# Optimization experiments

Hardware: AMD Instinct MI355X
Metric: run time of the kernel (lower is better)

## Reference

```python
import jax, jax.numpy as jnp
import numpy as np

N = 50000
E = 1600000
D_IN = 128
D_HID = 64
BN_EPS = 1e-5


def setup_inputs() -> dict:
    key = jax.random.key(0)
    ks = jax.random.split(key, 12)
    x = jax.random.normal(ks[0], (N, D_IN), dtype=jnp.float32)
    edge_index_sc = jax.random.randint(ks[1], (2, E), 0, N, dtype=jnp.int64)
    edge_weight_sc = jax.random.uniform(ks[2], (E,), dtype=jnp.float32)
    edge_index_fc = jax.random.randint(ks[3], (2, E), 0, N, dtype=jnp.int64)
    edge_weight_fc = jax.random.uniform(ks[4], (E,), dtype=jnp.float32)
    # learned parameters
    alpha = jnp.float32(0.5)
    W1 = jax.random.normal(ks[5], (D_IN, D_HID), dtype=jnp.float32) / np.sqrt(D_IN)
    b1 = jnp.zeros((D_HID,), dtype=jnp.float32)
    W2 = jax.random.normal(ks[6], (D_HID, D_HID), dtype=jnp.float32) / np.sqrt(D_HID)
    b2 = jnp.zeros((D_HID,), dtype=jnp.float32)
    gamma1 = jnp.ones((D_HID,), dtype=jnp.float32)
    beta1 = jnp.zeros((D_HID,), dtype=jnp.float32)
    gamma2 = jnp.ones((D_HID,), dtype=jnp.float32)
    beta2 = jnp.zeros((D_HID,), dtype=jnp.float32)
    return {"x": x, "edge_index_sc": edge_index_sc, "edge_weight_sc": edge_weight_sc,
            "edge_index_fc": edge_index_fc, "edge_weight_fc": edge_weight_fc,
            "alpha": alpha, "W1": W1, "b1": b1, "W2": W2, "b2": b2,
            "gamma1": gamma1, "beta1": beta1, "gamma2": gamma2, "beta2": beta2}


def _gcn_layer(h, W, b, src, dst, norm, n):
    # h: [N, d_in] -> [N, d_out]; PyG GCNConv: transform, then weighted scatter-add
    h = h @ W
    msg = h[src] * norm[:, None]                # [E+N, d_out] gather + scale
    out = jax.ops.segment_sum(msg, dst, num_segments=n)
    return out + b


def _bn_relu(h, gamma, beta):
    # BatchNorm1d (training-mode batch stats, biased variance) + ReLU
    mean = jnp.mean(h, axis=0)
    var = jnp.var(h, axis=0)
    h = (h - mean) * jax.lax.rsqrt(var + BN_EPS) * gamma + beta
    return jax.nn.relu(h)


def reference(x, edge_index_sc, edge_weight_sc, edge_index_fc, edge_weight_fc,
              alpha, W1, b1, W2, b2, gamma1, beta1, gamma2, beta2):
    n = x.shape[0]
    a = jax.nn.sigmoid(alpha)
    # mixed weights on SC topology (edge_index_fc unused, as in original)
    w_mix = a * edge_weight_sc + (1.0 - a) * edge_weight_fc
    # add self loops (weight 1) and compute symmetric GCN normalization
    loop = jnp.arange(n, dtype=edge_index_sc.dtype)
    src = jnp.concatenate([edge_index_sc[0], loop])
    dst = jnp.concatenate([edge_index_sc[1], loop])
    w = jnp.concatenate([w_mix, jnp.ones((n,), dtype=w_mix.dtype)])
    deg = jax.ops.segment_sum(w, dst, num_segments=n)
    dinv = jnp.where(deg > 0, jax.lax.rsqrt(jnp.maximum(deg, 1e-12)), 0.0)
    norm = dinv[src] * w * dinv[dst]
    h = _gcn_layer(x, W1, b1, src, dst, norm, n)
    h = _bn_relu(h, gamma1, beta1)
    h = _gcn_layer(h, W2, b2, src, dst, norm, n)
    h = _bn_relu(h, gamma2, beta2)
    return h  # dropout is identity in eval mode
```

## Files before the change

### kernel.cpp

```cpp
#include <hip/hip_runtime.h>
#include <hip/hip_fp16.h>
#include <math.h>

#define N_NODES 50000
#define N_EDGES 1600000
#define D_INF   128
#define D_HID   64
#define BN_EPS  1e-5f
#define NBINS   391
#define BINCAP  4608
#define EPB     6250
#define GEMM1B  3125
#define NPAIR   3125
#define NCOPY   64

struct SmGemm { float sw[D_INF * D_HID]; float sx[16 * D_INF]; };
struct SmBin  { int hcnt[NBINS]; int hbase[NBINS]; };
union SmPre { SmGemm g; SmBin a; };

__global__ __launch_bounds__(256) void k_pre(const float* __restrict__ wsc,
                                             const float* __restrict__ wfc,
                                             const int*   __restrict__ ei,
                                             const float* __restrict__ alpha,
                                             int* __restrict__ bin_cur,
                                             unsigned long long* __restrict__ binned,
                                             const float* __restrict__ x,
                                             const float* __restrict__ W,
                                             __half* __restrict__ ha,
                                             __half* __restrict__ hb) {
    __shared__ SmPre sm;
    int t = threadIdx.x;
    if (blockIdx.x < 256) {
        int e0 = blockIdx.x * EPB;
        for (int b = t; b < NBINS; b += 256) sm.a.hcnt[b] = 0;
        __syncthreads();
        for (int i = t; i < EPB; i += 256)
            atomicAdd(&sm.a.hcnt[ei[N_EDGES + e0 + i] >> 7], 1);
        __syncthreads();
        for (int b = t; b < NBINS; b += 256) {
            int c = sm.a.hcnt[b];
            sm.a.hbase[b] = c ? atomicAdd(&bin_cur[b], c) : 0;
            sm.a.hcnt[b] = 0;
        }
        __syncthreads();
        float a = 1.0f / (1.0f + expf(-alpha[0]));
        for (int i = t; i < EPB; i += 256) {
            int e = e0 + i;
            int s = ei[e], d = ei[N_EDGES + e];
            float wm = fmaf(a, wsc[e] - wfc[e], wfc[e]);
            int bin = d >> 7;
            int slot = atomicAdd(&sm.a.hcnt[bin], 1);
            int gpos = sm.a.hbase[bin] + slot;
            if (gpos < BINCAP) {
                unsigned long long ent =
                    ((unsigned long long)__float_as_uint(wm) << 32)
                    | (unsigned int)(s | ((d & 127) << 16));
                binned[(size_t)bin * BINCAP + gpos] = ent;
            }
        }
    } else {
        int row0 = (blockIdx.x - 256) * 16;
#pragma unroll
        for (int j = 0; j < 32; ++j) sm.g.sw[t + j * 256] = W[t + j * 256];
#pragma unroll
        for (int j = 0; j < 8; ++j) {
            int i = t + j * 256;
            int r = i >> 7, k = i & 127;
            sm.g.sx[i] = x[(row0 + r) * D_INF + k];
        }
        __syncthreads();
        int c = t & 63, rg = (t >> 6) * 4;
        float a0 = 0, a1 = 0, a2 = 0, a3 = 0;
#pragma unroll 4
        for (int k = 0; k < D_INF; ++k) {
            float w = sm.g.sw[k * D_HID + c];
            a0 = fmaf(sm.g.sx[(rg + 0) * D_INF + k], w, a0);
            a1 = fmaf(sm.g.sx[(rg + 1) * D_INF + k], w, a1);
            a2 = fmaf(sm.g.sx[(rg + 2) * D_INF + k], w, a2);
            a3 = fmaf(sm.g.sx[(rg + 3) * D_INF + k], w, a3);
        }
        __half* tbl = (c < 32) ? ha : hb;
        int cc = c & 31;
        tbl[(row0 + rg + 0) * 32 + cc] = __float2half_rn(a0);
        tbl[(row0 + rg + 1) * 32 + cc] = __float2half_rn(a1);
        tbl[(row0 + rg + 2) * 32 + cc] = __float2half_rn(a2);
        tbl[(row0 + rg + 3) * 32 + cc] = __float2half_rn(a3);
    }
}

__global__ __launch_bounds__(512) void k_binB(const int* __restrict__ bin_cur,
                                              const unsigned long long* __restrict__ binned,
                                              int2*  __restrict__ row_se,
                                              float* __restrict__ dinv,
                                              __half* __restrict__ ha,
                                              __half* __restrict__ hb,
                                              unsigned int* __restrict__ csr) {
    __shared__ unsigned long long stage[BINCAP];
    __shared__ unsigned long long nacc[128];
    __shared__ int   ncnt[128];
    __shared__ int   sscan[128];
    __shared__ float sdinv[128];
    __shared__ int   lb[128];
    int t = threadIdx.x;
    int bin = blockIdx.x;
    if (t < 128) nacc[t] = 0ULL;
    int cnt = min(bin_cur[bin], BINCAP);
    const unsigned long long* mybin = binned + (size_t)bin * BINCAP;
    for (int i = t; i < cnt; i += 512) stage[i] = mybin[i];
    __syncthreads();
    for (int i = t; i < cnt; i += 512) {
        unsigned long long ent = stage[i];
        unsigned int lo = (unsigned int)ent;
        int nl = (lo >> 16) & 127;
        float wm = __uint_as_float((unsigned int)(ent >> 32));
        unsigned long long pk = (1ULL << 48)
            | (unsigned long long)(wm * 4294967296.0f);
        atomicAdd(&nacc[nl], pk);
    }
    __syncthreads();
    int node0 = bin << 7;
    int nnodes = min(128, N_NODES - node0);
    if (t < 128) {
        unsigned long long v = nacc[t];
        int c = (int)(v >> 48);
        float nd = (float)(v & 0xFFFFFFFFFFFFULL) * 2.3283064365386963e-10f;
        float dv = rsqrtf(1.0f + nd);
        sdinv[t] = dv;
        if (t < nnodes) dinv[node0 + t] = dv;
        ncnt[t] = c;
        sscan[t] = c;
    }
    __syncthreads();
    for (int off = 1; off < 128; off <<= 1) {
        int u = (t >= off && t < 128) ? sscan[t - off] : 0;
        __syncthreads();
        if (t < 128) sscan[t] += u;
        __syncthreads();
    }
    if (t < nnodes) {
        int s = bin * BINCAP + sscan[t] - ncnt[t];
        row_se[node0 + t] = make_int2(s, s + ncnt[t]);
        lb[t] = s;
    }
    __syncthreads();
    int nh = nnodes * 16;
    __half2* pa = (__half2*)ha;
    __half2* pb = (__half2*)hb;
    for (int i = t; i < nh; i += 512) {
        int n = i >> 4;
        float dv = sdinv[n];
        int idx = node0 * 16 + i;
        float2 fa = __half22float2(pa[idx]);
        float2 fb = __half22float2(pb[idx]);
        pa[idx] = __floats2half2_rn(fa.x * dv, fa.y * dv);
        pb[idx] = __floats2half2_rn(fb.x * dv, fb.y * dv);
    }
    if (t < 128) ncnt[t] = 0;
    __syncthreads();
    for (int i = t; i < cnt; i += 512) {
        unsigned long long ent = stage[i];
        unsigned int lo = (unsigned int)ent;
        int nl  = (lo >> 16) & 127;
        int src = lo & 0xFFFFu;
        float wm = __uint_as_float((unsigned int)(ent >> 32));
        int slot = atomicAdd(&ncnt[nl], 1);
        unsigned short wh = __half_as_ushort(__float2half_rn(wm));
        csr[lb[nl] + slot] = (unsigned int)src | ((unsigned int)wh << 16);
    }
}

__device__ inline float hdec(unsigned int u) {
    return __half2float(__ushort_as_half((unsigned short)(u >> 16)));
}

__global__ __launch_bounds__(512) void k_gather(const __half* __restrict__ ha,
                                                const __half* __restrict__ hb,
                                                const unsigned int* __restrict__ csr,
                                                const int2*  __restrict__ row_se,
                                                const float* __restrict__ dinv,
                                                const float* __restrict__ bias,
                                                float* __restrict__ out,
                                                float* __restrict__ stat) {
    __shared__ float s1[512], s2[512];
    int t = threadIdx.x;
    int half = blockIdx.x & 1;
    const float4* __restrict__ h4 = (const float4*)(half ? hb : ha);
    int node = (blockIdx.x >> 1) * 16 + (t >> 5);
    int ln = t & 31;
    int sg = ln >> 2;
    int cq = ln & 3;
    int2 se = row_se[node];
    float dd = dinv[node];
    float acc[8];
    if (sg == 0) {
        float4 sv = h4[node * 4 + cq];
        const __half2* p = reinterpret_cast<const __half2*>(&sv);
#pragma unroll
        for (int i = 0; i < 4; ++i) {
            float2 f = __half22float2(p[i]);
            acc[2 * i] = f.x; acc[2 * i + 1] = f.y;
        }
    } else {
#pragma unroll
        for (int i = 0; i < 8; ++i) acc[i] = 0.0f;
    }
    for (int b = se.x; b < se.y; b += 32) {
        int c0 = min(32, se.y - b);
        int cm = c0 - 1;
        unsigned int my = (ln < c0) ? csr[b + ln] : 0u;
        unsigned int u0 = __shfl(my, min(sg,      cm), 32);
        unsigned int u1 = __shfl(my, min(sg + 8,  cm), 32);
        unsigned int u2 = __shfl(my, min(sg + 16, cm), 32);
        unsigned int u3 = __shfl(my, min(sg + 24, cm), 32);
        float4 r0 = h4[(u0 & 0xFFFFu) * 4 + cq];
        float4 r1 = h4[(u1 & 0xFFFFu) * 4 + cq];
        float4 r2 = h4[(u2 & 0xFFFFu) * 4 + cq];
        float4 r3 = h4[(u3 & 0xFFFFu) * 4 + cq];
        float w0 = (sg      < c0) ? hdec(u0) : 0.0f;
        float w1 = (sg + 8  < c0) ? hdec(u1) : 0.0f;
        float w2 = (sg + 16 < c0) ? hdec(u2) : 0.0f;
        float w3 = (sg + 24 < c0) ? hdec(u3) : 0.0f;
        const __half2* p0 = reinterpret_cast<const __half2*>(&r0);
        const __half2* p1 = reinterpret_cast<const __half2*>(&r1);
        const __half2* p2 = reinterpret_cast<const __half2*>(&r2);
        const __half2* p3 = reinterpret_cast<const __half2*>(&r3);
#pragma unroll
        for (int i = 0; i < 4; ++i) {
            float2 f0 = __half22float2(p0[i]);
            float2 f1 = __half22float2(p1[i]);
            float2 f2 = __half22float2(p2[i]);
            float2 f3 = __half22float2(p3[i]);
            acc[2*i]   = fmaf(f0.x, w0, acc[2*i]);
            acc[2*i+1] = fmaf(f0.y, w0, acc[2*i+1]);
            acc[2*i]   = fmaf(f1.x, w1, acc[2*i]);
            acc[2*i+1] = fmaf(f1.y, w1, acc[2*i+1]);
            acc[2*i]   = fmaf(f2.x, w2, acc[2*i]);
            acc[2*i+1] = fmaf(f2.y, w2, acc[2*i+1]);
            acc[2*i]   = fmaf(f3.x, w3, acc[2*i]);
            acc[2*i+1] = fmaf(f3.y, w3, acc[2*i+1]);
        }
    }
#pragma unroll
    for (int off = 16; off >= 4; off >>= 1) {
#pragma unroll
        for (int i = 0; i < 8; ++i) acc[i] += __shfl_down(acc[i], off, 32);
    }
    if (ln < 4) {
        int col0 = half * 32 + cq * 8;
        float v[8];
#pragma unroll
        for (int i = 0; i < 8; ++i) v[i] = fmaf(acc[i], dd, bias[col0 + i]);
        float4* o = (float4*)out;
        o[node * 16 + half * 8 + cq * 2]     = make_float4(v[0], v[1], v[2], v[3]);
        o[node * 16 + half * 8 + cq * 2 + 1] = make_float4(v[4], v[5], v[6], v[7]);
        int lb = (t >> 5) * 32 + cq * 8;
#pragma unroll
        for (int i = 0; i < 8; ++i) { s1[lb + i] = v[i]; s2[lb + i] = v[i] * v[i]; }
    }
    __syncthreads();
#pragma unroll
    for (int off = 256; off >= 32; off >>= 1) {
        if (t < off) { s1[t] += s1[t + off]; s2[t] += s2[t + off]; }
        __syncthreads();
    }
    if (t < 32) {
        int cp = (blockIdx.x >> 1) & (NCOPY - 1);
        int col = half * 32 + t;
        atomicAdd(&stat[cp * 128 + col],      s1[t]);
        atomicAdd(&stat[cp * 128 + 64 + col], s2[t]);
    }
}

__global__ __launch_bounds__(256) void k_gemm2_bn(const float* __restrict__ hin,
                                                  const float* __restrict__ stat,
                                                  const float* __restrict__ gamma,
                                                  const float* __restrict__ beta,
                                                  const float* __restrict__ W,
                                                  const float* __restrict__ dinv,
                                                  __half* __restrict__ ha,
                                                  __half* __restrict__ hb) {
    __shared__ float sw[D_HID * D_HID];
    __shared__ float sx[16 * D_HID];
    __shared__ float sc[D_HID], sh[D_HID];
    int t = threadIdx.x;
    int row0 = blockIdx.x * 16;
#pragma unroll
    for (int j = 0; j < 16; ++j) sw[t + j * 256] = W[t + j * 256];
    if (t < 64) {
        float s = 0.0f, q = 0.0f;
#pragma unroll 8
        for (int c = 0; c < NCOPY; ++c) {
            s += stat[c * 128 + t];
            q += stat[c * 128 + 64 + t];
        }
        const float invn = 1.0f / (float)N_NODES;
        float mean = s * invn;
        float var  = q * invn - mean * mean;
        float g    = gamma[t] * rsqrtf(var + BN_EPS);
        sc[t] = g;
        sh[t] = beta[t] - mean * g;
    }
    __syncthreads();
#pragma unroll
    for (int j = 0; j < 4; ++j) {
        int i = t + j * 256;
        int k = i & 63;
        sx[i] = fmaxf(0.0f, fmaf(hin[row0 * D_HID + i], sc[k], sh[k]));
    }
    __syncthreads();
    int c = t & 63, rg = (t >> 6) * 4;
    float a0 = 0, a1 = 0, a2 = 0, a3 = 0;
#pragma unroll 4
    for (int k = 0; k < D_HID; ++k) {
        float w = sw[k * D_HID + c];
        a0 = fmaf(sx[(rg + 0) * D_HID + k], w, a0);
        a1 = fmaf(sx[(rg + 1) * D_HID + k], w, a1);
        a2 = fmaf(sx[(rg + 2) * D_HID + k], w, a2);
        a3 = fmaf(sx[(rg + 3) * D_HID + k], w, a3);
    }
    __half* tbl = (c < 32) ? ha : hb;
    int cc = c & 31;
    tbl[(row0 + rg + 0) * 32 + cc] = __float2half_rn(a0 * dinv[row0 + rg + 0]);
    tbl[(row0 + rg + 1) * 32 + cc] = __float2half_rn(a1 * dinv[row0 + rg + 1]);
    tbl[(row0 + rg + 2) * 32 + cc] = __float2half_rn(a2 * dinv[row0 + rg + 2]);
    tbl[(row0 + rg + 3) * 32 + cc] = __float2half_rn(a3 * dinv[row0 + rg + 3]);
}

__global__ __launch_bounds__(256) void k_bn_apply_relu(float4* __restrict__ h,
                                                       const float* __restrict__ stat,
                                                       const float* __restrict__ gamma,
                                                       const float* __restrict__ beta) {
    __shared__ float sc[D_HID], sh[D_HID];
    int t = threadIdx.x;
    if (t < 64) {
        float s = 0.0f, q = 0.0f;
#pragma unroll 8
        for (int c = 0; c < NCOPY; ++c) {
            s += stat[c * 128 + t];
            q += stat[c * 128 + 64 + t];
        }
        const float invn = 1.0f / (float)N_NODES;
        float mean = s * invn;
        float var  = q * invn - mean * mean;
        float g    = gamma[t] * rsqrtf(var + BN_EPS);
        sc[t] = g;
        sh[t] = beta[t] - mean * g;
    }
    __syncthreads();
    int idx = blockIdx.x * 256 + t;
    if (idx >= N_NODES * D_HID / 4) return;
    int j = (idx & 15) * 4;
    float4 v = h[idx];
    v.x = fmaxf(0.0f, fmaf(v.x, sc[j],     sh[j]));
    v.y = fmaxf(0.0f, fmaf(v.y, sc[j + 1], sh[j + 1]));
    v.z = fmaxf(0.0f, fmaf(v.z, sc[j + 2], sh[j + 2]));
    v.w = fmaxf(0.0f, fmaf(v.w, sc[j + 3], sh[j + 3]));
    h[idx] = v;
}

extern "C" void kernel_launch(void* const* d_in, const int* in_sizes, int n_in,
                              void* d_out, int out_size, void* d_ws, size_t ws_size,
                              hipStream_t stream) {
    const float* x     = (const float*)d_in[0];
    const int*   ei_sc = (const int*)  d_in[1];
    const float* w_sc  = (const float*)d_in[2];
    const float* w_fc  = (const float*)d_in[4];
    const float* alpha = (const float*)d_in[5];
    const float* W1    = (const float*)d_in[6];
    const float* b1    = (const float*)d_in[7];
    const float* W2    = (const float*)d_in[8];
    const float* b2    = (const float*)d_in[9];
    const float* g1    = (const float*)d_in[10];
    const float* be1   = (const float*)d_in[11];
    const float* g2    = (const float*)d_in[12];
    const float* be2   = (const float*)d_in[13];
    float* out = (float*)d_out;

    unsigned long long* binned = (unsigned long long*)d_ws;
    int2*  row_se  = (int2*)(binned + (size_t)NBINS * BINCAP);
    int*   bin_cur = (int*)(row_se + N_NODES);
    float* stats   = (float*)(bin_cur + 400);
    float* dinv    = stats + 2 * NCOPY * 128;
    unsigned int* csr = (unsigned int*)(dinv + N_NODES);
    __half* ha     = (__half*)(csr + (size_t)NBINS * BINCAP);
    __half* hb     = ha + (size_t)N_NODES * 32;
    float* agg     = (float*)(hb + (size_t)N_NODES * 32);

    const int gV4 = (N_NODES * D_HID / 4 + 255) / 256;
    const int gGA = NPAIR * 2;
    const int gGM = N_NODES / 16;

    hipMemsetAsync(bin_cur, 0, (400 + 2 * NCOPY * 128) * sizeof(int), stream);
    k_pre <<<256 + GEMM1B, 256, 0, stream>>>(w_sc, w_fc, ei_sc, alpha,
                                             bin_cur, binned, x, W1, ha, hb);
    k_binB<<<NBINS, 512, 0, stream>>>(bin_cur, binned, row_se, dinv, ha, hb, csr);

    k_gather  <<<gGA, 512, 0, stream>>>(ha, hb, csr, row_se, dinv, b1, agg, stats);

    k_gemm2_bn<<<gGM, 256, 0, stream>>>(agg, stats, g1, be1, W2, dinv, ha, hb);
    k_gather  <<<gGA, 512, 0, stream>>>(ha, hb, csr, row_se, dinv, b2, out,
                                        stats + NCOPY * 128);
    k_bn_apply_relu<<<gV4, 256, 0, stream>>>((float4*)out, stats + NCOPY * 128,
                                             g2, be2);
}
```

Baseline: 276.6 us.

## Replace global-atomic edge binning with per-block fixed-capacity slot buckets

The edge binning pass drops its histogram pre-count and its global atomic bin cursors. Each block instead writes edges into a private fixed-capacity slot range per bin, stored as a 4-byte src/half-weight word plus a 1-byte local node id, and records per-block counts. The binning kernel then loads all slots of a bin into shared memory and skips the empty ones with the counts. The stats memset moves into the GEMM blocks of the pre kernel, and the aggregation buffer reuses the slot storage. Trade-offs: more shared memory and scanned slots per bin, edges silently dropped if a block exceeds 44 edges for one bin, and degrees now computed from half-rounded weights.

```diff
diff --git a/kernel.cpp b/kernel.cpp
--- a/kernel.cpp
+++ b/kernel.cpp
@@ -9,57 +9,61 @@
 #define BN_EPS  1e-5f
 #define NBINS   391
 #define BINCAP  4608
+#define CAPB    44
+#define SLOTS   (256 * CAPB)
 #define EPB     6250
 #define GEMM1B  3125
 #define NPAIR   3125
 #define NCOPY   64
 
 struct SmGemm { float sw[D_INF * D_HID]; float sx[16 * D_INF]; };
-struct SmBin  { int hcnt[NBINS]; int hbase[NBINS]; };
+struct SmBin  { int ncur[NBINS]; };
 union SmPre { SmGemm g; SmBin a; };
 
 __global__ __launch_bounds__(256) void k_pre(const float* __restrict__ wsc,
                                              const float* __restrict__ wfc,
                                              const int*   __restrict__ ei,
                                              const float* __restrict__ alpha,
-                                             int* __restrict__ bin_cur,
-                                             unsigned long long* __restrict__ binned,
+                                             unsigned short* __restrict__ cnt,
+                                             unsigned int*  __restrict__ b32,
+                                             unsigned char* __restrict__ b8,
                                              const float* __restrict__ x,
                                              const float* __restrict__ W,
                                              __half* __restrict__ ha,
-                                             __half* __restrict__ hb) {
+                                             __half* __restrict__ hb,
+                                             float* __restrict__ stats) {
     __shared__ SmPre sm;
     int t = threadIdx.x;
     if (blockIdx.x < 256) {
-        int e0 = blockIdx.x * EPB;
-        for (int b = t; b < NBINS; b += 256) sm.a.hcnt[b] = 0;
-        __syncthreads();
-        for (int i = t; i < EPB; i += 256)
-            atomicAdd(&sm.a.hcnt[ei[N_EDGES + e0 + i] >> 7], 1);
-        __syncthreads();
-        for (int b = t; b < NBINS; b += 256) {
-            int c = sm.a.hcnt[b];
-            sm.a.hbase[b] = c ? atomicAdd(&bin_cur[b], c) : 0;
-            sm.a.hcnt[b] = 0;
-        }
+        int blk = blockIdx.x;
+        for (int b = t; b < NBINS; b += 256) sm.a.ncur[b] = 0;
         __syncthreads();
         float a = 1.0f / (1.0f + expf(-alpha[0]));
+        int e0 = blk * EPB;
         for (int i = t; i < EPB; i += 256) {
             int e = e0 + i;
             int s = ei[e], d = ei[N_EDGES + e];
             float wm = fmaf(a, wsc[e] - wfc[e], wfc[e]);
             int bin = d >> 7;
-            int slot = atomicAdd(&sm.a.hcnt[bin], 1);
-            int gpos = sm.a.hbase[bin] + slot;
-            if (gpos < BINCAP) {
-                unsigned long long ent =
-                    ((unsigned long long)__float_as_uint(wm) << 32)
-                    | (unsigned int)(s | ((d & 127) << 16));
-                binned[(size_t)bin * BINCAP + gpos] = ent;
+            int slot = atomicAdd(&sm.a.ncur[bin], 1);
+            if (slot < CAPB) {
+                size_t p = (size_t)bin * SLOTS + blk * CAPB + slot;
+                unsigned short wh = __half_as_ushort(__float2half_rn(wm));
+                b32[p] = (unsigned int)s | ((unsigned int)wh << 16);
+                b8[p]  = (unsigned char)(d & 127);
             }
         }
+        __syncthreads();
+        for (int b = t; b < NBINS; b += 256)
+            cnt[blk * NBINS + b] = (unsigned short)min(sm.a.ncur[b], CAPB);
     } else {
-        int row0 = (blockIdx.x - 256) * 16;
+        int gb = blockIdx.x - 256;
+        if (gb < 32) {
+            int o = gb * 512 + t;
+            stats[o] = 0.0f;
+            stats[o + 256] = 0.0f;
+        }
+        int row0 = gb * 16;
 #pragma unroll
         for (int j = 0; j < 32; ++j) sm.g.sw[t + j * 256] = W[t + j * 256];
 #pragma unroll
@@ -88,34 +92,43 @@
     }
 }
 
-__global__ __launch_bounds__(512) void k_binB(const int* __restrict__ bin_cur,
-                                              const unsigned long long* __restrict__ binned,
+__global__ __launch_bounds__(512) void k_binB(const unsigned short* __restrict__ cnt,
+                                              const unsigned int*  __restrict__ b32,
+                                              const unsigned char* __restrict__ b8,
                                               int2*  __restrict__ row_se,
                                               float* __restrict__ dinv,
                                               __half* __restrict__ ha,
                                               __half* __restrict__ hb,
                                               unsigned int* __restrict__ csr) {
-    __shared__ unsigned long long stage[BINCAP];
+    __shared__ unsigned int  st32[SLOTS];
+    __shared__ unsigned char st8[SLOTS];
+    __shared__ unsigned short scnt[256];
     __shared__ unsigned long long nacc[128];
     __shared__ int   ncnt[128];
     __shared__ int   sscan[128];
+    __shared__ int   lb[128];
     __shared__ float sdinv[128];
-    __shared__ int   lb[128];
     int t = threadIdx.x;
     int bin = blockIdx.x;
+    if (t < 256) scnt[t] = cnt[t * NBINS + bin];
     if (t < 128) nacc[t] = 0ULL;
-    int cnt = min(bin_cur[bin], BINCAP);
-    const unsigned long long* mybin = binned + (size_t)bin * BINCAP;
-    for (int i = t; i < cnt; i += 512) stage[i] = mybin[i];
-    __syncthreads();
-    for (int i = t; i < cnt; i += 512) {
-        unsigned long long ent = stage[i];
-        unsigned int lo = (unsigned int)ent;
-        int nl = (lo >> 16) & 127;
-        float wm = __uint_as_float((unsigned int)(ent >> 32));
-        unsigned long long pk = (1ULL << 48)
-            | (unsigned long long)(wm * 4294967296.0f);
-        atomicAdd(&nacc[nl], pk);
+    size_t base = (size_t)bin * SLOTS;
+    {
+        const uint4* g4 = (const uint4*)(b32 + base);
+        uint4* s4 = (uint4*)st32;
+        for (int i = t; i < SLOTS / 4; i += 512) s4[i] = g4[i];
+        const unsigned int* g1 = (const unsigned int*)(b8 + base);
+        unsigned int* s1w = (unsigned int*)st8;
+        for (int i = t; i < SLOTS / 4; i += 512) s1w[i] = g1[i];
+    }
+    __syncthreads();
+    for (int i = t; i < SLOTS; i += 512) {
+        int seg = i / CAPB;
+        if (i - seg * CAPB < (int)scnt[seg]) {
+            float wm = __half2float(__ushort_as_half((unsigned short)(st32[i] >> 16)));
+            atomicAdd(&nacc[st8[i]],
+                      (1ULL << 48) | (unsigned long long)(wm * 4294967296.0f));
+        }
     }
     __syncthreads();
     int node0 = bin << 7;
@@ -137,10 +150,14 @@
         if (t < 128) sscan[t] += u;
         __syncthreads();
     }
-    if (t < nnodes) {
-        int s = bin * BINCAP + sscan[t] - ncnt[t];
-        row_se[node0 + t] = make_int2(s, s + ncnt[t]);
-        lb[t] = s;
+    if (t < 128) {
+        int l = sscan[t] - ncnt[t];
+        lb[t] = l;
+        if (t < nnodes) {
+            int s0 = min(l, BINCAP);
+            int s1 = min(l + ncnt[t], BINCAP);
+            row_se[node0 + t] = make_int2(bin * BINCAP + s0, bin * BINCAP + s1);
+        }
     }
     __syncthreads();
     int nh = nnodes * 16;
@@ -157,15 +174,14 @@
     }
     if (t < 128) ncnt[t] = 0;
     __syncthreads();
-    for (int i = t; i < cnt; i += 512) {
-        unsigned long long ent = stage[i];
-        unsigned int lo = (unsigned int)ent;
-        int nl  = (lo >> 16) & 127;
-        int src = lo & 0xFFFFu;
-        float wm = __uint_as_float((unsigned int)(ent >> 32));
-        int slot = atomicAdd(&ncnt[nl], 1);
-        unsigned short wh = __half_as_ushort(__float2half_rn(wm));
-        csr[lb[nl] + slot] = (unsigned int)src | ((unsigned int)wh << 16);
+    for (int i = t; i < SLOTS; i += 512) {
+        int seg = i / CAPB;
+        if (i - seg * CAPB < (int)scnt[seg]) {
+            int nl = st8[i];
+            int slot = atomicAdd(&ncnt[nl], 1);
+            int pos = lb[nl] + slot;
+            if (pos < BINCAP) csr[bin * BINCAP + pos] = st32[i];
+        }
     }
 }
 
@@ -253,9 +269,9 @@
         float4* o = (float4*)out;
         o[node * 16 + half * 8 + cq * 2]     = make_float4(v[0], v[1], v[2], v[3]);
         o[node * 16 + half * 8 + cq * 2 + 1] = make_float4(v[4], v[5], v[6], v[7]);
-        int lb = (t >> 5) * 32 + cq * 8;
-#pragma unroll
-        for (int i = 0; i < 8; ++i) { s1[lb + i] = v[i]; s2[lb + i] = v[i] * v[i]; }
+        int lbx = (t >> 5) * 32 + cq * 8;
+#pragma unroll
+        for (int i = 0; i < 8; ++i) { s1[lbx + i] = v[i]; s2[lbx + i] = v[i] * v[i]; }
     }
     __syncthreads();
 #pragma unroll
@@ -376,24 +392,25 @@
     const float* be2   = (const float*)d_in[13];
     float* out = (float*)d_out;
 
-    unsigned long long* binned = (unsigned long long*)d_ws;
-    int2*  row_se  = (int2*)(binned + (size_t)NBINS * BINCAP);
-    int*   bin_cur = (int*)(row_se + N_NODES);
-    float* stats   = (float*)(bin_cur + 400);
-    float* dinv    = stats + 2 * NCOPY * 128;
-    unsigned int* csr = (unsigned int*)(dinv + N_NODES);
-    __half* ha     = (__half*)(csr + (size_t)NBINS * BINCAP);
-    __half* hb     = ha + (size_t)N_NODES * 32;
-    float* agg     = (float*)(hb + (size_t)N_NODES * 32);
+    const size_t NSLOT = (size_t)NBINS * SLOTS;
+    unsigned int* b32 = (unsigned int*)d_ws;
+    float* agg = (float*)d_ws;
+    unsigned int* csr = b32 + NSLOT;
+    __half* ha  = (__half*)(csr + (size_t)NBINS * BINCAP);
+    __half* hb  = ha + (size_t)N_NODES * 32;
+    int2*  row_se = (int2*)(hb + (size_t)N_NODES * 32);
+    float* dinv   = (float*)(row_se + N_NODES);
+    float* stats  = dinv + N_NODES;
+    unsigned short* cnt = (unsigned short*)(stats + 2 * NCOPY * 128);
+    unsigned char* b8 = (unsigned char*)(cnt + 256 * NBINS);
 
     const int gV4 = (N_NODES * D_HID / 4 + 255) / 256;
     const int gGA = NPAIR * 2;
     const int gGM = N_NODES / 16;
 
-    hipMemsetAsync(bin_cur, 0, (400 + 2 * NCOPY * 128) * sizeof(int), stream);
     k_pre <<<256 + GEMM1B, 256, 0, stream>>>(w_sc, w_fc, ei_sc, alpha,
-                                             bin_cur, binned, x, W1, ha, hb);
-    k_binB<<<NBINS, 512, 0, stream>>>(bin_cur, binned, row_se, dinv, ha, hb, csr);
+                                             cnt, b32, b8, x, W1, ha, hb, stats);
+    k_binB<<<NBINS, 512, 0, stream>>>(cnt, b32, b8, row_se, dinv, ha, hb, csr);
 
     k_gather  <<<gGA, 512, 0, stream>>>(ha, hb, csr, row_se, dinv, b1, agg, stats);
 
```

After: 296.5 us. +7.2%, slower.
